# Performance work log

Measured on AMD Instinct MI355X. Metric: run time of the kernel, lower is better.

## Reference

```python
import jax, jax.numpy as jnp
import numpy as np

N = 50000      # nodes
E = 800000     # directed edges (avg degree 16)
F_IN = 128     # dataset.num_features
H = 256        # hidden_channels
C = 40         # dataset.num_classes


def _glorot(k, shape):
    lim = float(np.sqrt(6.0 / (shape[0] + shape[1])))
    return jax.random.uniform(k, shape, jnp.float32, -lim, lim)


def setup_inputs() -> dict:
    key = jax.random.key(0)
    ks = jax.random.split(key, 8)
    x = jax.random.normal(ks[0], (N, F_IN), jnp.float32)
    edge_index = jax.random.randint(ks[1], (2, E), 0, N, dtype=jnp.int32)
    W1 = _glorot(ks[2], (F_IN, H));      b1 = jnp.zeros((H,), jnp.float32)
    W2 = _glorot(ks[3], (H, H // 2));    b2 = jnp.zeros((H // 2,), jnp.float32)
    W3 = _glorot(ks[4], (H // 2, H // 4)); b3 = jnp.zeros((H // 4,), jnp.float32)
    W4 = _glorot(ks[5], (H // 4, C));    b4 = jnp.zeros((C,), jnp.float32)
    return {"x": x, "edge_index": edge_index,
            "W1": W1, "b1": b1, "W2": W2, "b2": b2,
            "W3": W3, "b3": b3, "W4": W4, "b4": b4}


def reference(x, edge_index, W1, b1, W2, b2, W3, b3, W4, b4):
    # GCNConv with default add_self_loops=True and symmetric normalization.
    loops = jnp.arange(N, dtype=edge_index.dtype)
    src = jnp.concatenate([edge_index[0], loops])   # message sources
    dst = jnp.concatenate([edge_index[1], loops])   # aggregation targets
    # degree computed on target index (PyG default), incl. self-loops
    deg = jax.ops.segment_sum(jnp.ones_like(dst, jnp.float32), dst, num_segments=N)
    dinv = jnp.where(deg > 0, jax.lax.rsqrt(deg), 0.0)
    norm = dinv[src] * dinv[dst]                    # [E+N]

    def conv(h, W, b):
        h = h @ W                                   # transform first (PyG order)
        msg = h[src] * norm[:, None]                # gather + scale
        return jax.ops.segment_sum(msg, dst, num_segments=N) + b

    h = jax.nn.relu(conv(x, W1, b1))   # dropout = identity in eval mode
    h = jax.nn.relu(conv(h, W2, b2))
    h = jax.nn.relu(conv(h, W3, b3))
    return conv(h, W4, b4)
```

## Files before the change

kernel.cpp:

```cpp
#include <hip/hip_runtime.h>
#include <stdint.h>

#define NNODES 50000
#define NEDGES 800000
#define NB ((NNODES + 255) / 256)
#define EPB 4096
#define SCAT_NBLK ((NEDGES + EPB - 1) / EPB)

typedef __attribute__((ext_vector_type(8))) short bf16x8;
typedef __attribute__((ext_vector_type(4))) float f32x4;

__device__ inline unsigned short f2bf(float f) {
    unsigned u = __float_as_uint(f);
    return (unsigned short)((u + 0x7fffu + ((u >> 16) & 1u)) >> 16);
}
__device__ inline float bf2f(unsigned short h) {
    return __uint_as_float(((unsigned)h) << 16);
}


template <int K, int M>
__device__ inline void repack_body(const float* __restrict__ W,
                                   unsigned short* __restrict__ hi,
                                   unsigned short* __restrict__ lo, int blk) {
    const int i = blk * 256 + threadIdx.x;
    const int k = i / M, n = i % M;
    constexpr int KS = K / 32;
    const int cb = n >> 7;
    const int ct = (n >> 4) & 7;
    const int ln = ((k >> 3) & 3) * 16 + (n & 15);
    const int j  = k & 7;
    const int ks = k >> 5;
    const size_t o = ((((size_t)cb * KS + ks) * 8 + ct) * 64 + ln) * 8 + j;
    const float f = W[i];
    const unsigned short h = f2bf(f);
    hi[o] = h;
    lo[o] = f2bf(f - bf2f(h));
}

__global__ __launch_bounds__(256) void prep_kernel(const float* __restrict__ W1,
                                                   unsigned short* __restrict__ W1hi,
                                                   unsigned short* __restrict__ W1lo,
                                                   const float* __restrict__ W2,
                                                   unsigned short* __restrict__ W2hi,
                                                   unsigned short* __restrict__ W2lo,
                                                   int* __restrict__ bhist) {
    const int b = blockIdx.x;
    if (b < 128) repack_body<128, 256>(W1, W1hi, W1lo, b);
    else if (b < 256) repack_body<256, 128>(W2, W2hi, W2lo, b - 128);
    else if (threadIdx.x < NB) bhist[threadIdx.x] = 0;
}


__global__ __launch_bounds__(256) void bucket_count_kernel(const int* __restrict__ dst,
                                                           int* __restrict__ bhist) {
    __shared__ int h[NB];
    for (int b = threadIdx.x; b < NB; b += 256) h[b] = 0;
    __syncthreads();
    const int base = blockIdx.x * EPB;
#pragma unroll
    for (int i = 0; i < EPB / 256; ++i) {
        const int e = base + threadIdx.x + i * 256;
        if (e < NEDGES) atomicAdd(&h[dst[e] >> 8], 1);
    }
    __syncthreads();
    for (int b = threadIdx.x; b < NB; b += 256)
        if (h[b]) atomicAdd(&bhist[b], h[b]);
}

__global__ __launch_bounds__(256) void bucket_scan_kernel(const int* __restrict__ bhist,
                                                          int* __restrict__ bofs,
                                                          int* __restrict__ gcur,
                                                          int* __restrict__ rp_last) {
    __shared__ int s[256];
    const int t = threadIdx.x;
    s[t] = (t < NB) ? bhist[t] : 0;
    __syncthreads();
    for (int off = 1; off < 256; off <<= 1) {
        int v = (t >= off) ? s[t - off] : 0;
        __syncthreads();
        s[t] += v;
        __syncthreads();
    }
    if (t < NB) {
        const int excl = (t > 0) ? s[t - 1] : 0;
        bofs[t] = excl;
        gcur[t] = excl;
    }
    if (t == 255) { bofs[NB] = s[255]; rp_last[0] = s[255]; }
}

__global__ __launch_bounds__(256) void bucket_scatter_kernel(const int* __restrict__ src,
                                                             const int* __restrict__ dst,
                                                             int* __restrict__ gcur,
                                                             unsigned* __restrict__ gpk) {
    __shared__ int h[256];
    __shared__ int s[256];
    __shared__ int gof[256];
    __shared__ unsigned pr[EPB];
    __shared__ int ga[EPB];

    const int t = threadIdx.x;
    const int base = blockIdx.x * EPB;
    const int nval = min(EPB, NEDGES - base);

    h[t] = 0;
    __syncthreads();
#pragma unroll
    for (int i = 0; i < EPB / 256; ++i) {
        const int e = base + t + i * 256;
        if (e < NEDGES) atomicAdd(&h[dst[e] >> 8], 1);
    }
    __syncthreads();
    s[t] = h[t];
    __syncthreads();
    for (int off = 1; off < 256; off <<= 1) {
        int v = (t >= off) ? s[t - off] : 0;
        __syncthreads();
        s[t] += v;
        __syncthreads();
    }
    {
        const int c = h[t];
        if (t < NB && c > 0) gof[t] = atomicAdd(&gcur[t], c);
        const int lofs = s[t] - c;
        h[t] = lofs;
        s[t] = lofs;
    }
    __syncthreads();
#pragma unroll
    for (int i = 0; i < EPB / 256; ++i) {
        const int e = base + t + i * 256;
        if (e < NEDGES) {
            const int d = dst[e];
            const int b = d >> 8;
            const int slot = atomicAdd(&h[b], 1);
            pr[slot] = ((unsigned)(d & 255) << 16) | (unsigned)src[e];
            ga[slot] = gof[b] + (slot - s[b]);
        }
    }
    __syncthreads();
#pragma unroll
    for (int i = 0; i < EPB / 256; ++i) {
        const int slot = t + i * 256;
        if (slot < nval) gpk[ga[slot]] = pr[slot];
    }
}

__global__ __launch_bounds__(256) void csr_fill_kernel(const unsigned* __restrict__ gpk,
                                                       const int* __restrict__ bofs,
                                                       int* __restrict__ rp,
                                                       float* __restrict__ dinv,
                                                       unsigned short* __restrict__ col,
                                                       const float* __restrict__ x,
                                                       unsigned short* __restrict__ xbf) {
    __shared__ int c[256];
    __shared__ int s[256];
    __shared__ int cur[256];
    __shared__ float dvv[256];
    const int t = threadIdx.x;
    const int b = blockIdx.x;
    const int beg = bofs[b], end = bofs[b + 1];
    c[t] = 0;
    __syncthreads();
    for (int e = beg + t; e < end; e += 256) atomicAdd(&c[gpk[e] >> 16], 1);
    __syncthreads();
    s[t] = c[t];
    __syncthreads();
    for (int off = 1; off < 256; off <<= 1) {
        int v = (t >= off) ? s[t - off] : 0;
        __syncthreads();
        s[t] += v;
        __syncthreads();
    }
    const int excl = s[t] - c[t];
    cur[t] = excl;
    const int node = b * 256 + t;
    const float dv = rsqrtf((float)(c[t] + 1));
    dvv[t] = dv;
    if (node < NNODES) {
        rp[node] = beg + excl;
        dinv[node] = dv;
    }
    __syncthreads();
    for (int e = beg + t; e < end; e += 256) {
        const unsigned p = gpk[e];
        const int r = atomicAdd(&cur[p >> 16], 1);
        col[beg + r] = (unsigned short)(p & 0xffffu);
    }
#pragma unroll
    for (int i = 0; i < 32; ++i) {
        const int idx = t + i * 256;
        const int row = idx >> 5;
        const int g = idx & 31;
        const int nd = b * 256 + row;
        if (nd < NNODES) {
            const float dvr = dvv[row];
            float4 v = *(const float4*)(x + (size_t)nd * 128 + g * 4);
            ushort4 h;
            h.x = f2bf(dvr * v.x); h.y = f2bf(dvr * v.y);
            h.z = f2bf(dvr * v.z); h.w = f2bf(dvr * v.w);
            *(ushort4*)(xbf + (size_t)nd * 128 + g * 4) = h;
        }
    }
}


template <bool RELU, bool HAS_BIAS>
__global__ __launch_bounds__(256) void agg128_kernel(const float* __restrict__ in32,
                                                     const unsigned short* __restrict__ inbf,
                                                     float* __restrict__ out,
                                                     const int* __restrict__ rp,
                                                     const unsigned short* __restrict__ col,
                                                     const float* __restrict__ dinv,
                                                     const float* __restrict__ bias) {
    const int wave = threadIdx.x >> 6;
    const int lane = threadIdx.x & 63;
    const int d = blockIdx.x * 4 + wave;
    if (d >= NNODES) return;
    const int half = lane >> 5;
    const int fl = lane & 31;
    const float dv = dinv[d];

    float acc[4] = {0.f, 0.f, 0.f, 0.f};
    if (half == 0) {
        float4 s = *(const float4*)(in32 + (size_t)d * 128 + fl * 4);
        acc[0] = dv * s.x; acc[1] = dv * s.y; acc[2] = dv * s.z; acc[3] = dv * s.w;
    }

    int j = rp[d] + half;
    const int end = rp[d + 1];
    for (; j + 6 < end; j += 8) {
        const int c0 = col[j], c1 = col[j + 2], c2 = col[j + 4], c3 = col[j + 6];
        ushort4 a0 = *(const ushort4*)(inbf + (size_t)c0 * 128 + fl * 4);
        ushort4 a1 = *(const ushort4*)(inbf + (size_t)c1 * 128 + fl * 4);
        ushort4 a2 = *(const ushort4*)(inbf + (size_t)c2 * 128 + fl * 4);
        ushort4 a3 = *(const ushort4*)(inbf + (size_t)c3 * 128 + fl * 4);
        acc[0] += (bf2f(a0.x) + bf2f(a1.x)) + (bf2f(a2.x) + bf2f(a3.x));
        acc[1] += (bf2f(a0.y) + bf2f(a1.y)) + (bf2f(a2.y) + bf2f(a3.y));
        acc[2] += (bf2f(a0.z) + bf2f(a1.z)) + (bf2f(a2.z) + bf2f(a3.z));
        acc[3] += (bf2f(a0.w) + bf2f(a1.w)) + (bf2f(a2.w) + bf2f(a3.w));
    }
    for (; j < end; j += 2) {
        const int c0 = col[j];
        ushort4 a0 = *(const ushort4*)(inbf + (size_t)c0 * 128 + fl * 4);
        acc[0] += bf2f(a0.x); acc[1] += bf2f(a0.y); acc[2] += bf2f(a0.z); acc[3] += bf2f(a0.w);
    }

#pragma unroll
    for (int v = 0; v < 4; ++v) acc[v] += __shfl_down(acc[v], 32);

    if (half == 0) {
        float4 r;
        float* pr = &r.x;
#pragma unroll
        for (int v = 0; v < 4; ++v) {
            float t = dv * acc[v];
            if constexpr (HAS_BIAS) t += bias[fl * 4 + v];
            if constexpr (RELU) t = fmaxf(t, 0.0f);
            pr[v] = t;
        }
        *(float4*)(out + (size_t)d * 128 + fl * 4) = r;
    }
}

template <bool RELU, bool HAS_BIAS, bool WRITE_BF>
__global__ __launch_bounds__(256) void agg64_kernel(const float* __restrict__ in32,
                                                    const unsigned short* __restrict__ inbf,
                                                    float* __restrict__ out,
                                                    unsigned short* __restrict__ outbf,
                                                    const int* __restrict__ rp,
                                                    const unsigned short* __restrict__ col,
                                                    const float* __restrict__ dinv,
                                                    const float* __restrict__ bias) {
    const int wave = threadIdx.x >> 6;
    const int lane = threadIdx.x & 63;
    const int d = blockIdx.x * 4 + wave;
    if (d >= NNODES) return;
    const int quarter = lane >> 4;
    const int fl = lane & 15;
    const float dv = dinv[d];

    float acc[4] = {0.f, 0.f, 0.f, 0.f};
    if (quarter == 0) {
        float4 s = *(const float4*)(in32 + (size_t)d * 64 + fl * 4);
        acc[0] = dv * s.x; acc[1] = dv * s.y; acc[2] = dv * s.z; acc[3] = dv * s.w;
    }

    int j = rp[d] + quarter;
    const int end = rp[d + 1];
    for (; j + 12 < end; j += 16) {
        const int c0 = col[j], c1 = col[j + 4], c2 = col[j + 8], c3 = col[j + 12];
        ushort4 a0 = *(const ushort4*)(inbf + (size_t)c0 * 64 + fl * 4);
        ushort4 a1 = *(const ushort4*)(inbf + (size_t)c1 * 64 + fl * 4);
        ushort4 a2 = *(const ushort4*)(inbf + (size_t)c2 * 64 + fl * 4);
        ushort4 a3 = *(const ushort4*)(inbf + (size_t)c3 * 64 + fl * 4);
        acc[0] += (bf2f(a0.x) + bf2f(a1.x)) + (bf2f(a2.x) + bf2f(a3.x));
        acc[1] += (bf2f(a0.y) + bf2f(a1.y)) + (bf2f(a2.y) + bf2f(a3.y));
        acc[2] += (bf2f(a0.z) + bf2f(a1.z)) + (bf2f(a2.z) + bf2f(a3.z));
        acc[3] += (bf2f(a0.w) + bf2f(a1.w)) + (bf2f(a2.w) + bf2f(a3.w));
    }
    for (; j < end; j += 4) {
        const int c0 = col[j];
        ushort4 a0 = *(const ushort4*)(inbf + (size_t)c0 * 64 + fl * 4);
        acc[0] += bf2f(a0.x); acc[1] += bf2f(a0.y); acc[2] += bf2f(a0.z); acc[3] += bf2f(a0.w);
    }

#pragma unroll
    for (int v = 0; v < 4; ++v) {
        acc[v] += __shfl_down(acc[v], 32);
        acc[v] += __shfl_down(acc[v], 16);
    }

    if (quarter == 0) {
        float4 r;
        float* pr = &r.x;
#pragma unroll
        for (int v = 0; v < 4; ++v) {
            float t = dv * acc[v];
            if constexpr (HAS_BIAS) t += bias[fl * 4 + v];
            if constexpr (RELU) t = fmaxf(t, 0.0f);
            pr[v] = t;
        }
        *(float4*)(out + (size_t)d * 64 + fl * 4) = r;
        if constexpr (WRITE_BF) {
            ushort4 hb;
            hb.x = f2bf(dv * pr[0]); hb.y = f2bf(dv * pr[1]);
            hb.z = f2bf(dv * pr[2]); hb.w = f2bf(dv * pr[3]);
            *(ushort4*)(outbf + (size_t)d * 64 + fl * 4) = hb;
        }
    }
}


template <int K, int M, int BM, bool BIAS_RELU, bool WRITE_BF>
__global__ __launch_bounds__(256) void mfma_gemm_kernel(const float* __restrict__ A,
                                                        const unsigned short* __restrict__ Whi,
                                                        const unsigned short* __restrict__ Wlo,
                                                        const float* __restrict__ bias,
                                                        float* __restrict__ C,
                                                        unsigned short* __restrict__ Cbf,
                                                        const float* __restrict__ dinv) {
    constexpr int KS = K / 32;
    constexpr int ASZ = BM * 64;
    constexpr int CI = (BM == 128) ? 4 : 2;
    __shared__ char lds[2 * ASZ + 16384];
    char* Ahi = lds;
    char* Alo = lds + ASZ;
    char* Bhi = lds + 2 * ASZ;
    char* Blo = lds + 2 * ASZ + 8192;

    const int t = threadIdx.x;
    const int lane = t & 63;
    const int w = t >> 6;
    const int wr = (BM == 128) ? (w >> 1) : 0;
    const int wc = (BM == 128) ? (w & 1) : w;
    const int r0 = blockIdx.x * BM;
    const int n0 = blockIdx.y * 128;

    const unsigned short* bhg = Whi + (size_t)blockIdx.y * KS * 4096;
    const unsigned short* blg = Wlo + (size_t)blockIdx.y * KS * 4096;

    f32x4 acc[4][CI];
#pragma unroll
    for (int i = 0; i < 4; ++i)
#pragma unroll
        for (int j = 0; j < CI; ++j) acc[i][j] = (f32x4){0.f, 0.f, 0.f, 0.f};

    for (int ks = 0; ks < KS; ++ks) {
        const int k0 = ks * 32;

        {
            const char* gh = (const char*)(bhg + (size_t)ks * 4096);
            const char* gl = (const char*)(blg + (size_t)ks * 4096);
#pragma unroll
            for (int c = 0; c < 2; ++c) {
                const int ct = w * 2 + c;
                __builtin_amdgcn_global_load_lds(
                    (const __attribute__((address_space(1))) void*)(gh + ct * 1024 + lane * 16),
                    (__attribute__((address_space(3))) void*)(Bhi + ct * 1024), 16, 0, 0);
                __builtin_amdgcn_global_load_lds(
                    (const __attribute__((address_space(1))) void*)(gl + ct * 1024 + lane * 16),
                    (__attribute__((address_space(3))) void*)(Blo + ct * 1024), 16, 0, 0);
            }
        }

        float4 av[BM / 32];
#pragma unroll
        for (int i = 0; i < BM / 32; ++i) {
            const int q = t + i * 256;
            const int row = q >> 3;
            const int kq = (q & 7) * 4;
            const int gr = r0 + row;
            float4 v = make_float4(0.f, 0.f, 0.f, 0.f);
            if (gr < NNODES) v = *(const float4*)(A + (size_t)gr * K + k0 + kq);
            av[i] = v;
        }
#pragma unroll
        for (int i = 0; i < BM / 32; ++i) {
            const int q = t + i * 256;
            const int row = q >> 3;
            const int kq = (q & 7) * 4;
            const int rt = row >> 4, m = row & 15, quad = kq >> 3, j0 = kq & 7;
            const int off = rt * 1024 + (quad * 16 + m) * 16 + j0 * 2;
            const float4 v = av[i];
            ushort4 h, l;
            h.x = f2bf(v.x); l.x = f2bf(v.x - bf2f(h.x));
            h.y = f2bf(v.y); l.y = f2bf(v.y - bf2f(h.y));
            h.z = f2bf(v.z); l.z = f2bf(v.z - bf2f(h.z));
            h.w = f2bf(v.w); l.w = f2bf(v.w - bf2f(h.w));
            *(ushort4*)(Ahi + off) = h;
            *(ushort4*)(Alo + off) = l;
        }
        __syncthreads();

        bf16x8 ah[4], al[4], bh[CI], bl[CI];
#pragma unroll
        for (int i = 0; i < 4; ++i) {
            ah[i] = *(const bf16x8*)(Ahi + (wr * 4 + i) * 1024 + lane * 16);
            al[i] = *(const bf16x8*)(Alo + (wr * 4 + i) * 1024 + lane * 16);
        }
#pragma unroll
        for (int j = 0; j < CI; ++j) {
            bh[j] = *(const bf16x8*)(Bhi + (wc * CI + j) * 1024 + lane * 16);
            bl[j] = *(const bf16x8*)(Blo + (wc * CI + j) * 1024 + lane * 16);
        }
#pragma unroll
        for (int i = 0; i < 4; ++i)
#pragma unroll
            for (int j = 0; j < CI; ++j) {
                acc[i][j] = __builtin_amdgcn_mfma_f32_16x16x32_bf16(ah[i], bh[j], acc[i][j], 0, 0, 0);
                acc[i][j] = __builtin_amdgcn_mfma_f32_16x16x32_bf16(ah[i], bl[j], acc[i][j], 0, 0, 0);
                acc[i][j] = __builtin_amdgcn_mfma_f32_16x16x32_bf16(al[i], bh[j], acc[i][j], 0, 0, 0);
            }
        __syncthreads();
    }

    const int quad = lane >> 4;
    const int cl = lane & 15;
#pragma unroll
    for (int i = 0; i < 4; ++i) {
#pragma unroll
        for (int j = 0; j < CI; ++j) {
            const int colg = n0 + wc * (CI * 16) + j * 16 + cl;
            float bv = 0.f;
            if constexpr (BIAS_RELU) bv = bias[colg];
#pragma unroll
            for (int r = 0; r < 4; ++r) {
                const int rowg = r0 + wr * 64 + i * 16 + quad * 4 + r;
                if (rowg < NNODES) {
                    float v = acc[i][j][r] + bv;
                    if constexpr (BIAS_RELU) v = fmaxf(v, 0.f);
                    C[(size_t)rowg * M + colg] = v;
                    if constexpr (WRITE_BF) Cbf[(size_t)rowg * M + colg] = f2bf(dinv[rowg] * v);
                }
            }
        }
    }
}


template <int BM, int BN, int BK, int TM, int TN, bool HAS_BIAS, bool RELU, bool WRITE_BF>
__global__ __launch_bounds__(256) void gemm_kernel(const float* __restrict__ A,
                                                   const float* __restrict__ W,
                                                   const float* __restrict__ bias,
                                                   float* __restrict__ C,
                                                   unsigned short* __restrict__ Cbf,
                                                   const float* __restrict__ dinv,
                                                   int Nrows, int K, int M) {
    constexpr int TX = BN / TN;
    constexpr int TY = BM / TM;
    static_assert(TX * TY == 256, "thread grid must be 256");
    constexpr int A_LOADS = (BM * BK) / (256 * 4);
    constexpr int W_LOADS = (BN * BK) / (256 * 4);
    static_assert(A_LOADS >= 1 && W_LOADS >= 1, "tile too small");

    const int tid = threadIdx.x;
    const int tx = tid % TX;
    const int ty = tid / TX;
    const int r0 = blockIdx.x * BM;
    const int c0 = blockIdx.y * BN;

    __shared__ float As[BK][BM + 4];
    __shared__ float Ws[BK][BN];

    float acc[TM][TN] = {};

    for (int k0 = 0; k0 < K; k0 += BK) {
#pragma unroll
        for (int l = 0; l < A_LOADS; ++l) {
            const int idx = tid + l * 256;
            const int row = idx / (BK / 4);
            const int kq = idx % (BK / 4);
            float4 v = make_float4(0.f, 0.f, 0.f, 0.f);
            const int gr = r0 + row;
            if (gr < Nrows) v = *(const float4*)(A + (size_t)gr * K + k0 + kq * 4);
            As[kq * 4 + 0][row] = v.x;
            As[kq * 4 + 1][row] = v.y;
            As[kq * 4 + 2][row] = v.z;
            As[kq * 4 + 3][row] = v.w;
        }
#pragma unroll
        for (int l = 0; l < W_LOADS; ++l) {
            const int idx = tid + l * 256;
            const int kk = idx / (BN / 4);
            const int cq = idx % (BN / 4);
            const int gc = c0 + cq * 4;
            float4 v;
            const float* wrow = W + (size_t)(k0 + kk) * M;
            if (gc + 3 < M) {
                v = *(const float4*)(wrow + gc);
            } else {
                v.x = (gc + 0 < M) ? wrow[gc + 0] : 0.f;
                v.y = (gc + 1 < M) ? wrow[gc + 1] : 0.f;
                v.z = (gc + 2 < M) ? wrow[gc + 2] : 0.f;
                v.w = (gc + 3 < M) ? wrow[gc + 3] : 0.f;
            }
            *(float4*)&Ws[kk][cq * 4] = v;
        }
        __syncthreads();

#pragma unroll
        for (int kk = 0; kk < BK; ++kk) {
            float a[TM], b[TN];
#pragma unroll
            for (int i = 0; i < TM; ++i) a[i] = As[kk][ty * TM + i];
#pragma unroll
            for (int j = 0; j < TN; ++j) b[j] = Ws[kk][tx * TN + j];
#pragma unroll
            for (int i = 0; i < TM; ++i)
#pragma unroll
                for (int j = 0; j < TN; ++j) acc[i][j] += a[i] * b[j];
        }
        __syncthreads();
    }

#pragma unroll
    for (int i = 0; i < TM; ++i) {
        const int gr = r0 + ty * TM + i;
        if (gr >= Nrows) continue;
        const float dvr = WRITE_BF ? dinv[gr] : 0.f;
#pragma unroll
        for (int j = 0; j < TN; ++j) {
            const int gc = c0 + tx * TN + j;
            if (gc >= M) continue;
            float v = acc[i][j];
            if constexpr (HAS_BIAS) v += bias[gc];
            if constexpr (RELU) v = fmaxf(v, 0.0f);
            C[(size_t)gr * M + gc] = v;
            if constexpr (WRITE_BF) Cbf[(size_t)gr * M + gc] = f2bf(dvr * v);
        }
    }
}


extern "C" void kernel_launch(void* const* d_in, const int* in_sizes, int n_in,
                              void* d_out, int out_size, void* d_ws, size_t ws_size,
                              hipStream_t stream) {
    const float* x  = (const float*)d_in[0];
    const int* ei   = (const int*)d_in[1];
    const float* W1 = (const float*)d_in[2];
    const float* b1 = (const float*)d_in[3];
    const float* W2 = (const float*)d_in[4];
    const float* b2 = (const float*)d_in[5];
    const float* W3 = (const float*)d_in[6];
    const float* b3 = (const float*)d_in[7];
    const float* W4 = (const float*)d_in[8];
    const float* b4 = (const float*)d_in[9];
    float* out = (float*)d_out;
    const int* esrc = ei;
    const int* edst = ei + NEDGES;

    char* w = (char*)d_ws;
    auto alloc = [&](size_t bytes) -> void* {
        void* p = (void*)w;
        w += (bytes + 255) & ~(size_t)255;
        return p;
    };
    int* rp     = (int*)alloc((size_t)(NNODES + 1) * 4);
    unsigned short* col = (unsigned short*)alloc((size_t)NEDGES * 2);
    float* dinv = (float*)alloc((size_t)NNODES * 4);
    int* bhist  = (int*)alloc((size_t)NB * 4);
    int* bofs   = (int*)alloc((size_t)(NB + 1) * 4);
    int* gcur   = (int*)alloc((size_t)NB * 4);
    unsigned* gpk = (unsigned*)alloc((size_t)NEDGES * 4);
    unsigned short* W1hi = (unsigned short*)alloc((size_t)128 * 256 * 2);
    unsigned short* W1lo = (unsigned short*)alloc((size_t)128 * 256 * 2);
    unsigned short* W2hi = (unsigned short*)alloc((size_t)256 * 128 * 2);
    unsigned short* W2lo = (unsigned short*)alloc((size_t)256 * 128 * 2);
    float* B0   = (float*)alloc((size_t)NNODES * 256 * 4);
    float* B1   = (float*)alloc((size_t)NNODES * 128 * 4);
    float* B2   = (float*)alloc((size_t)NNODES * 128 * 4);
    unsigned short* xbf  = (unsigned short*)alloc((size_t)NNODES * 128 * 2);
    unsigned short* B1bf = (unsigned short*)alloc((size_t)NNODES * 128 * 2);
    unsigned short* B0bf = (unsigned short*)alloc((size_t)NNODES * 64 * 2);
    unsigned short* B3bf = (unsigned short*)alloc((size_t)NNODES * 64 * 2);

    prep_kernel<<<257, 256, 0, stream>>>(W1, W1hi, W1lo, W2, W2hi, W2lo, bhist);

    bucket_count_kernel<<<SCAT_NBLK, 256, 0, stream>>>(edst, bhist);
    bucket_scan_kernel<<<1, 256, 0, stream>>>(bhist, bofs, gcur, rp + NNODES);
    bucket_scatter_kernel<<<SCAT_NBLK, 256, 0, stream>>>(esrc, edst, gcur, gpk);
    csr_fill_kernel<<<NB, 256, 0, stream>>>(gpk, bofs, rp, dinv, col, x, xbf);

    const int aggGrid = (NNODES + 3) / 4;
    const int rowBlks64 = (NNODES + 63) / 64;

    agg128_kernel<false, false><<<aggGrid, 256, 0, stream>>>(x, xbf, B2, rp, col, dinv, nullptr);
    mfma_gemm_kernel<128, 256, 64, true, false>
        <<<dim3(rowBlks64, 2), 256, 0, stream>>>(B2, W1hi, W1lo, b1, B0, nullptr, nullptr);

    mfma_gemm_kernel<256, 128, 64, false, true>
        <<<dim3(rowBlks64, 1), 256, 0, stream>>>(B0, W2hi, W2lo, nullptr, B1, B1bf, dinv);
    agg128_kernel<true, true><<<aggGrid, 256, 0, stream>>>(B1, B1bf, B2, rp, col, dinv, b2);

    gemm_kernel<64, 64, 16, 4, 4, false, false, true>
        <<<dim3(rowBlks64, 1), 256, 0, stream>>>(B2, W3, nullptr, B0, B0bf, dinv, NNODES, 128, 64);
    agg64_kernel<true, true, true><<<aggGrid, 256, 0, stream>>>(B0, B0bf, B1, B3bf, rp, col, dinv, b3);

    agg64_kernel<false, false, false><<<aggGrid, 256, 0, stream>>>(B1, B3bf, B2, nullptr, rp, col, dinv, nullptr);
    gemm_kernel<64, 64, 16, 4, 4, true, false, false>
        <<<dim3(rowBlks64, 1), 256, 0, stream>>>(B2, W4, b4, out, nullptr, nullptr, NNODES, 64, 40);
}
```

Measured before the change: 358.4 us.

## Chunk bf16 message buffers into 16-feature column blocks for cache-local gathers

Stores the bf16 gather sources in a chunked layout, with a [F/16][N][16] slab per 16-feature group, and rewrites aggregation as one kernel that processes one feature chunk per block. Block index bits interleave chunks so that concurrent blocks gather from a small 1.6MB slab that can stay in cache. The aim is to cut random-access DRAM traffic and improve L2 hit rate. The cost is more blocks, narrower 4-byte loads per lane, an extra shuffle reduction level, and re-reading the CSR indices once per chunk.

```diff
diff --git a/kernel.cpp b/kernel.cpp
--- a/kernel.cpp
+++ b/kernel.cpp
@@ -200,134 +200,76 @@
             ushort4 h;
             h.x = f2bf(dvr * v.x); h.y = f2bf(dvr * v.y);
             h.z = f2bf(dvr * v.z); h.w = f2bf(dvr * v.w);
-            *(ushort4*)(xbf + (size_t)nd * 128 + g * 4) = h;
-        }
-    }
-}
-
-
-template <bool RELU, bool HAS_BIAS>
-__global__ __launch_bounds__(256) void agg128_kernel(const float* __restrict__ in32,
-                                                     const unsigned short* __restrict__ inbf,
-                                                     float* __restrict__ out,
-                                                     const int* __restrict__ rp,
-                                                     const unsigned short* __restrict__ col,
-                                                     const float* __restrict__ dinv,
-                                                     const float* __restrict__ bias) {
+            const size_t o = ((size_t)(g >> 2) * NNODES + nd) * 16 + (g & 3) * 4;
+            *(ushort4*)(xbf + o) = h;
+        }
+    }
+}
+
+
+template <int F, bool RELU, bool HAS_BIAS, bool WRITE_BF>
+__global__ __launch_bounds__(256) void aggc_kernel(const float* __restrict__ in32,
+                                                   const unsigned short* __restrict__ inbf,
+                                                   float* __restrict__ out,
+                                                   unsigned short* __restrict__ outbf,
+                                                   const int* __restrict__ rp,
+                                                   const unsigned short* __restrict__ col,
+                                                   const float* __restrict__ dinv,
+                                                   const float* __restrict__ bias) {
+    constexpr int CF = 16;
+    constexpr int NCHUNK = F / CF;
+    constexpr int SUBS = 8 / NCHUNK;
+    const int B = blockIdx.x;
+    const int x = B & 7;
+    const int chunk = x / SUBS;
+    const int sub = x % SUBS;
     const int wave = threadIdx.x >> 6;
     const int lane = threadIdx.x & 63;
-    const int d = blockIdx.x * 4 + wave;
+    const int d = ((B >> 3) * SUBS + sub) * 4 + wave;
     if (d >= NNODES) return;
-    const int half = lane >> 5;
-    const int fl = lane & 31;
+    const int eg = lane >> 3;
+    const int fl = lane & 7;
     const float dv = dinv[d];
 
-    float acc[4] = {0.f, 0.f, 0.f, 0.f};
-    if (half == 0) {
-        float4 s = *(const float4*)(in32 + (size_t)d * 128 + fl * 4);
-        acc[0] = dv * s.x; acc[1] = dv * s.y; acc[2] = dv * s.z; acc[3] = dv * s.w;
-    }
-
-    int j = rp[d] + half;
+    const unsigned short* mbase = inbf + (size_t)chunk * NNODES * CF + fl * 2;
+
+    float a0 = 0.f, a1 = 0.f;
+    if (eg == 0) {
+        float2 s = *(const float2*)(in32 + (size_t)d * F + chunk * CF + fl * 2);
+        a0 = dv * s.x; a1 = dv * s.y;
+    }
+
+    int j = rp[d] + eg;
     const int end = rp[d + 1];
-    for (; j + 6 < end; j += 8) {
-        const int c0 = col[j], c1 = col[j + 2], c2 = col[j + 4], c3 = col[j + 6];
-        ushort4 a0 = *(const ushort4*)(inbf + (size_t)c0 * 128 + fl * 4);
-        ushort4 a1 = *(const ushort4*)(inbf + (size_t)c1 * 128 + fl * 4);
-        ushort4 a2 = *(const ushort4*)(inbf + (size_t)c2 * 128 + fl * 4);
-        ushort4 a3 = *(const ushort4*)(inbf + (size_t)c3 * 128 + fl * 4);
-        acc[0] += (bf2f(a0.x) + bf2f(a1.x)) + (bf2f(a2.x) + bf2f(a3.x));
-        acc[1] += (bf2f(a0.y) + bf2f(a1.y)) + (bf2f(a2.y) + bf2f(a3.y));
-        acc[2] += (bf2f(a0.z) + bf2f(a1.z)) + (bf2f(a2.z) + bf2f(a3.z));
-        acc[3] += (bf2f(a0.w) + bf2f(a1.w)) + (bf2f(a2.w) + bf2f(a3.w));
-    }
-    for (; j < end; j += 2) {
-        const int c0 = col[j];
-        ushort4 a0 = *(const ushort4*)(inbf + (size_t)c0 * 128 + fl * 4);
-        acc[0] += bf2f(a0.x); acc[1] += bf2f(a0.y); acc[2] += bf2f(a0.z); acc[3] += bf2f(a0.w);
-    }
-
-#pragma unroll
-    for (int v = 0; v < 4; ++v) acc[v] += __shfl_down(acc[v], 32);
-
-    if (half == 0) {
-        float4 r;
-        float* pr = &r.x;
-#pragma unroll
-        for (int v = 0; v < 4; ++v) {
-            float t = dv * acc[v];
-            if constexpr (HAS_BIAS) t += bias[fl * 4 + v];
-            if constexpr (RELU) t = fmaxf(t, 0.0f);
-            pr[v] = t;
-        }
-        *(float4*)(out + (size_t)d * 128 + fl * 4) = r;
-    }
-}
-
-template <bool RELU, bool HAS_BIAS, bool WRITE_BF>
-__global__ __launch_bounds__(256) void agg64_kernel(const float* __restrict__ in32,
-                                                    const unsigned short* __restrict__ inbf,
-                                                    float* __restrict__ out,
-                                                    unsigned short* __restrict__ outbf,
-                                                    const int* __restrict__ rp,
-                                                    const unsigned short* __restrict__ col,
-                                                    const float* __restrict__ dinv,
-                                                    const float* __restrict__ bias) {
-    const int wave = threadIdx.x >> 6;
-    const int lane = threadIdx.x & 63;
-    const int d = blockIdx.x * 4 + wave;
-    if (d >= NNODES) return;
-    const int quarter = lane >> 4;
-    const int fl = lane & 15;
-    const float dv = dinv[d];
-
-    float acc[4] = {0.f, 0.f, 0.f, 0.f};
-    if (quarter == 0) {
-        float4 s = *(const float4*)(in32 + (size_t)d * 64 + fl * 4);
-        acc[0] = dv * s.x; acc[1] = dv * s.y; acc[2] = dv * s.z; acc[3] = dv * s.w;
-    }
-
-    int j = rp[d] + quarter;
-    const int end = rp[d + 1];
-    for (; j + 12 < end; j += 16) {
-        const int c0 = col[j], c1 = col[j + 4], c2 = col[j + 8], c3 = col[j + 12];
-        ushort4 a0 = *(const ushort4*)(inbf + (size_t)c0 * 64 + fl * 4);
-        ushort4 a1 = *(const ushort4*)(inbf + (size_t)c1 * 64 + fl * 4);
-        ushort4 a2 = *(const ushort4*)(inbf + (size_t)c2 * 64 + fl * 4);
-        ushort4 a3 = *(const ushort4*)(inbf + (size_t)c3 * 64 + fl * 4);
-        acc[0] += (bf2f(a0.x) + bf2f(a1.x)) + (bf2f(a2.x) + bf2f(a3.x));
-        acc[1] += (bf2f(a0.y) + bf2f(a1.y)) + (bf2f(a2.y) + bf2f(a3.y));
-        acc[2] += (bf2f(a0.z) + bf2f(a1.z)) + (bf2f(a2.z) + bf2f(a3.z));
-        acc[3] += (bf2f(a0.w) + bf2f(a1.w)) + (bf2f(a2.w) + bf2f(a3.w));
-    }
-    for (; j < end; j += 4) {
-        const int c0 = col[j];
-        ushort4 a0 = *(const ushort4*)(inbf + (size_t)c0 * 64 + fl * 4);
-        acc[0] += bf2f(a0.x); acc[1] += bf2f(a0.y); acc[2] += bf2f(a0.z); acc[3] += bf2f(a0.w);
-    }
-
-#pragma unroll
-    for (int v = 0; v < 4; ++v) {
-        acc[v] += __shfl_down(acc[v], 32);
-        acc[v] += __shfl_down(acc[v], 16);
-    }
-
-    if (quarter == 0) {
-        float4 r;
-        float* pr = &r.x;
-#pragma unroll
-        for (int v = 0; v < 4; ++v) {
-            float t = dv * acc[v];
-            if constexpr (HAS_BIAS) t += bias[fl * 4 + v];
-            if constexpr (RELU) t = fmaxf(t, 0.0f);
-            pr[v] = t;
-        }
-        *(float4*)(out + (size_t)d * 64 + fl * 4) = r;
+    for (; j + 8 < end; j += 16) {
+        const int c0 = col[j], c1 = col[j + 8];
+        const unsigned v0 = *(const unsigned*)(mbase + (size_t)c0 * CF);
+        const unsigned v1 = *(const unsigned*)(mbase + (size_t)c1 * CF);
+        a0 += bf2f((unsigned short)(v0 & 0xffffu)) + bf2f((unsigned short)(v1 & 0xffffu));
+        a1 += bf2f((unsigned short)(v0 >> 16)) + bf2f((unsigned short)(v1 >> 16));
+    }
+    if (j < end) {
+        const unsigned v0 = *(const unsigned*)(mbase + (size_t)col[j] * CF);
+        a0 += bf2f((unsigned short)(v0 & 0xffffu));
+        a1 += bf2f((unsigned short)(v0 >> 16));
+    }
+
+    a0 += __shfl_down(a0, 32); a1 += __shfl_down(a1, 32);
+    a0 += __shfl_down(a0, 16); a1 += __shfl_down(a1, 16);
+    a0 += __shfl_down(a0, 8);  a1 += __shfl_down(a1, 8);
+
+    if (eg == 0) {
+        float t0 = dv * a0, t1 = dv * a1;
+        if constexpr (HAS_BIAS) {
+            t0 += bias[chunk * CF + fl * 2];
+            t1 += bias[chunk * CF + fl * 2 + 1];
+        }
+        if constexpr (RELU) { t0 = fmaxf(t0, 0.f); t1 = fmaxf(t1, 0.f); }
+        *(float2*)(out + (size_t)d * F + chunk * CF + fl * 2) = make_float2(t0, t1);
         if constexpr (WRITE_BF) {
-            ushort4 hb;
-            hb.x = f2bf(dv * pr[0]); hb.y = f2bf(dv * pr[1]);
-            hb.z = f2bf(dv * pr[2]); hb.w = f2bf(dv * pr[3]);
-            *(ushort4*)(outbf + (size_t)d * 64 + fl * 4) = hb;
+            ushort2 hb;
+            hb.x = f2bf(dv * t0); hb.y = f2bf(dv * t1);
+            *(ushort2*)(outbf + ((size_t)chunk * NNODES + d) * CF + fl * 2) = hb;
         }
     }
 }
@@ -452,7 +394,9 @@
                     float v = acc[i][j][r] + bv;
                     if constexpr (BIAS_RELU) v = fmaxf(v, 0.f);
                     C[(size_t)rowg * M + colg] = v;
-                    if constexpr (WRITE_BF) Cbf[(size_t)rowg * M + colg] = f2bf(dinv[rowg] * v);
+                    if constexpr (WRITE_BF)
+                        Cbf[((size_t)(colg >> 4) * NNODES + rowg) * 16 + (colg & 15)] =
+                            f2bf(dinv[rowg] * v);
                 }
             }
         }
@@ -548,7 +492,8 @@
             if constexpr (HAS_BIAS) v += bias[gc];
             if constexpr (RELU) v = fmaxf(v, 0.0f);
             C[(size_t)gr * M + gc] = v;
-            if constexpr (WRITE_BF) Cbf[(size_t)gr * M + gc] = f2bf(dvr * v);
+            if constexpr (WRITE_BF)
+                Cbf[((size_t)(gc >> 4) * NNODES + gr) * 16 + (gc & 15)] = f2bf(dvr * v);
         }
     }
 }
@@ -603,22 +548,27 @@
     bucket_scatter_kernel<<<SCAT_NBLK, 256, 0, stream>>>(esrc, edst, gcur, gpk);
     csr_fill_kernel<<<NB, 256, 0, stream>>>(gpk, bofs, rp, dinv, col, x, xbf);
 
-    const int aggGrid = (NNODES + 3) / 4;
+    const int aggGrid128 = (NNODES / 4) * 8;
+    const int aggGrid64  = (NNODES / 8) * 8;
     const int rowBlks64 = (NNODES + 63) / 64;
 
-    agg128_kernel<false, false><<<aggGrid, 256, 0, stream>>>(x, xbf, B2, rp, col, dinv, nullptr);
+    aggc_kernel<128, false, false, false>
+        <<<aggGrid128, 256, 0, stream>>>(x, xbf, B2, nullptr, rp, col, dinv, nullptr);
     mfma_gemm_kernel<128, 256, 64, true, false>
         <<<dim3(rowBlks64, 2), 256, 0, stream>>>(B2, W1hi, W1lo, b1, B0, nullptr, nullptr);
 
     mfma_gemm_kernel<256, 128, 64, false, true>
         <<<dim3(rowBlks64, 1), 256, 0, stream>>>(B0, W2hi, W2lo, nullptr, B1, B1bf, dinv);
-    agg128_kernel<true, true><<<aggGrid, 256, 0, stream>>>(B1, B1bf, B2, rp, col, dinv, b2);
+    aggc_kernel<128, true, true, false>
+        <<<aggGrid128, 256, 0, stream>>>(B1, B1bf, B2, nullptr, rp, col, dinv, b2);
 
     gemm_kernel<64, 64, 16, 4, 4, false, false, true>
         <<<dim3(rowBlks64, 1), 256, 0, stream>>>(B2, W3, nullptr, B0, B0bf, dinv, NNODES, 128, 64);
-    agg64_kernel<true, true, true><<<aggGrid, 256, 0, stream>>>(B0, B0bf, B1, B3bf, rp, col, dinv, b3);
-
-    agg64_kernel<false, false, false><<<aggGrid, 256, 0, stream>>>(B1, B3bf, B2, nullptr, rp, col, dinv, nullptr);
+    aggc_kernel<64, true, true, true>
+        <<<aggGrid64, 256, 0, stream>>>(B0, B0bf, B1, B3bf, rp, col, dinv, b3);
+
+    aggc_kernel<64, false, false, false>
+        <<<aggGrid64, 256, 0, stream>>>(B1, B3bf, B2, nullptr, rp, col, dinv, nullptr);
     gemm_kernel<64, 64, 16, 4, 4, true, false, false>
         <<<dim3(rowBlks64, 1), 256, 0, stream>>>(B2, W4, b4, out, nullptr, nullptr, NNODES, 64, 40);
 }
```

Measured after the change: 561.8 us. +56.8%, slower.
